# Kernel tuning notes

Measured on AMD Instinct MI355X. Metric: run time of the kernel, lower is better.

The kernel has to match this reference:

```python
import jax, jax.numpy as jnp
import numpy as np

B, T, E, H = 8, 1024, 256, 8
TEMP = E ** 0.5


def setup_inputs() -> dict:
    key = jax.random.key(0)
    ks = jax.random.split(key, 7)
    x = jax.random.normal(ks[0], (B, T, E), dtype=jnp.float32)
    # boolean mask: True = masked position (masked_fill with -inf)
    mask = jax.random.randint(ks[1], (B, T, T), 0, 2) > 0
    s_in = 1.0 / np.sqrt(E)
    s_fc = 1.0 / np.sqrt(H * E)
    Wq = jax.random.normal(ks[2], (E, H * E), dtype=jnp.float32) * s_in
    Wk = jax.random.normal(ks[3], (E, H * E), dtype=jnp.float32) * s_in
    Wv = jax.random.normal(ks[4], (E, H * E), dtype=jnp.float32) * s_in
    Wfc = jax.random.normal(ks[5], (H * E, E), dtype=jnp.float32) * s_fc
    bfc = jax.random.normal(ks[6], (E,), dtype=jnp.float32) * s_fc
    return {"x": x, "Wq": Wq, "Wk": Wk, "Wv": Wv, "Wfc": Wfc, "bfc": bfc, "mask": mask}


def reference(x, Wq, Wk, Wv, Wfc, bfc, mask):
    b, t, e = x.shape
    h = H
    # QKV projections -> [b, t, h, e] (per-head dim == emb_dim here)
    q = (x @ Wq).reshape(b, t, h, e)
    k = (x @ Wk).reshape(b, t, h, e)
    v = (x @ Wv).reshape(b, t, h, e)
    # scores: [b, h, q, k]
    attn = jnp.einsum('bqhe,bkhe->bhqk', q / TEMP, k)
    attn = jnp.where(mask[:, None, :, :], -jnp.inf, attn)
    attn = jax.nn.softmax(attn, axis=-1)
    # rows fully masked give NaN -> replaced by 0 (masked_fill(attn != attn, 0))
    attn = jnp.where(jnp.isnan(attn), 0.0, attn)
    out = jnp.einsum('bhqk,bkhe->bqhe', attn, v).reshape(b, t, h * e)
    return out @ Wfc + bfc
```

## Files before the change

kernel.cpp:

```cpp
#include <hip/hip_runtime.h>


typedef __attribute__((ext_vector_type(8))) short bf16x8;
typedef __attribute__((ext_vector_type(4))) float f32x4;
typedef __attribute__((ext_vector_type(4))) unsigned short u16x4;
typedef __attribute__((ext_vector_type(2))) unsigned int u32x2;
typedef __attribute__((ext_vector_type(4))) int i32x4;

#define B_DIM 8
#define T_DIM 1024
#define E_DIM 256
#define H_DIM 8

__device__ __forceinline__ unsigned short f2bf(float f) {
  unsigned u = __builtin_bit_cast(unsigned, f);
  u += 0x7FFFu + ((u >> 16) & 1u);
  return (unsigned short)(u >> 16);
}

__device__ __forceinline__ void gload_lds16(const void* g, void* l) {
  __builtin_amdgcn_global_load_lds(
      (const __attribute__((address_space(1))) void*)g,
      (__attribute__((address_space(3))) void*)l, 16, 0, 0);
}

__device__ __forceinline__ f32x4 mfma16(bf16x8 a, bf16x8 b, f32x4 c) {
  return __builtin_amdgcn_mfma_f32_16x16x32_bf16(a, b, c, 0, 0, 0);
}

__global__ __launch_bounds__(256) void prep_all(
    const float* __restrict__ x, unsigned short* __restrict__ xbf,
    const int* __restrict__ mask, unsigned* __restrict__ mpk,
    const float* __restrict__ Wq, const float* __restrict__ Wk,
    const float* __restrict__ Wv, const float* __restrict__ Wfc,
    unsigned short* __restrict__ wall, unsigned short* __restrict__ wfcT) {
  __shared__ unsigned short tile[64][65];
  const int bid = blockIdx.x, tid = threadIdx.x;
  if (bid < 2048) {
    int i = bid * 256 + tid;
    f32x4 v = ((const f32x4*)x)[i];
    u16x4 o = { f2bf(v[0]), f2bf(v[1]), f2bf(v[2]), f2bf(v[3]) };
    ((u16x4*)xbf)[i] = o;
    return;
  }
  if (bid < 3072) {
    int i = (bid - 2048) * 256 + tid;
    const i32x4* src = (const i32x4*)(mask + (size_t)i * 32);
    unsigned v = 0;
#pragma unroll
    for (int j = 0; j < 8; ++j) {
      i32x4 a = src[j];
      v |= (a[0] != 0 ? 1u : 0u) << (j * 4 + 0);
      v |= (a[1] != 0 ? 1u : 0u) << (j * 4 + 1);
      v |= (a[2] != 0 ? 1u : 0u) << (j * 4 + 2);
      v |= (a[3] != 0 ? 1u : 0u) << (j * 4 + 3);
    }
    mpk[i] = v;
    return;
  }
  const int which = (bid - 3072) >> 7, bx = (bid - 3072) & 127;
  const float* in;
  unsigned short* out;
  int K, N, n0, k0;
  float scale;
  if (which < 3) {
    in = which == 0 ? Wq : (which == 1 ? Wk : Wv);
    out = wall + (size_t)which * 2048 * 256;
    K = 256; N = 2048; scale = which == 2 ? 1.0f : 0.25f;
    n0 = (bx & 31) * 64; k0 = (bx >> 5) * 64;
  } else {
    in = Wfc; out = wfcT; K = 2048; N = 256; scale = 1.0f;
    n0 = (bx & 3) * 64; k0 = (bx >> 2) * 64;
  }
#pragma unroll
  for (int p = 0; p < 16; ++p) {
    int i = p * 256 + tid;
    int r = i >> 6, c = i & 63;
    tile[c][r] = f2bf(in[(size_t)(k0 + r) * N + n0 + c] * scale);
  }
  __syncthreads();
#pragma unroll
  for (int p = 0; p < 16; ++p) {
    int i = p * 256 + tid;
    int r = i >> 6, c = i & 63;
    out[(size_t)(n0 + r) * K + k0 + c] = tile[r][c];
  }
}

__global__ __launch_bounds__(512) void gemm_qkv(
    const unsigned short* __restrict__ A, const unsigned short* __restrict__ BT,
    unsigned short* __restrict__ qk, unsigned short* __restrict__ vout) {
  __shared__ unsigned short As[256 * 64];
  __shared__ unsigned short Bs[128 * 64];
  const int tid = threadIdx.x;
  const int w = tid >> 6, l = tid & 63, lg = l >> 4, lr = l & 15;
  const int tn = blockIdx.x * 128, tm = blockIdx.y * 256;
  const int wm = (w >> 1) * 64, wn = (w & 1) * 64;

  f32x4 acc[4][4];
#pragma unroll
  for (int i = 0; i < 4; ++i)
#pragma unroll
    for (int j = 0; j < 4; ++j) acc[i][j] = (f32x4){0.f, 0.f, 0.f, 0.f};

  for (int kt = 0; kt < 256; kt += 64) {
#pragma unroll
    for (int j = 0; j < 4; ++j) {
      int d = j * 8192 + tid * 16;
      int row = d >> 7, cb = d & 127;
      gload_lds16((const char*)(A + (size_t)(tm + row) * 256 + kt) + (cb ^ ((row & 7) << 4)),
                  (char*)As + d);
    }
#pragma unroll
    for (int j = 0; j < 2; ++j) {
      int d = j * 8192 + tid * 16;
      int row = d >> 7, cb = d & 127;
      gload_lds16((const char*)(BT + (size_t)(tn + row) * 256 + kt) + (cb ^ ((row & 7) << 4)),
                  (char*)Bs + d);
    }
    __syncthreads();
#pragma unroll
    for (int c = 0; c < 2; ++c) {
      bf16x8 af[4], bfr[4];
#pragma unroll
      for (int mf = 0; mf < 4; ++mf) {
        int row = wm + mf * 16 + lr;
        af[mf] = *(const bf16x8*)((const char*)As + row * 128 +
                                  ((c * 64 + lg * 16) ^ ((row & 7) << 4)));
      }
#pragma unroll
      for (int nf = 0; nf < 4; ++nf) {
        int row = wn + nf * 16 + lr;
        bfr[nf] = *(const bf16x8*)((const char*)Bs + row * 128 +
                                   ((c * 64 + lg * 16) ^ ((row & 7) << 4)));
      }
#pragma unroll
      for (int mf = 0; mf < 4; ++mf)
#pragma unroll
        for (int nf = 0; nf < 4; ++nf)
          acc[mf][nf] = mfma16(af[mf], bfr[nf], acc[mf][nf]);
    }
    __syncthreads();
  }

  if (tn < 4096) {
#pragma unroll
    for (int mf = 0; mf < 4; ++mf)
#pragma unroll
      for (int nf = 0; nf < 4; ++nf) {
        int col = tn + wn + nf * 16 + lr;
        int row0 = tm + wm + mf * 16 + lg * 4;
        int h16 = col >> 8, e = col & 255;
#pragma unroll
        for (int r = 0; r < 4; ++r) {
          int rowm = row0 + r;
          int bi = rowm >> 10, t = rowm & 1023;
          qk[(((size_t)bi * 16 + h16) * T_DIM + t) * E_DIM + e] = f2bf(acc[mf][nf][r]);
        }
      }
  } else {
#pragma unroll
    for (int mf = 0; mf < 4; ++mf)
#pragma unroll
      for (int nf = 0; nf < 4; ++nf) {
        int col = tn + wn + nf * 16 + lr;
        int row0 = tm + wm + mf * 16 + lg * 4;
        int bi = row0 >> 10, t0 = row0 & 1023;
        int hh = (col >> 8) - 16, e = col & 255;
        u16x4 pk = { f2bf(acc[mf][nf][0]), f2bf(acc[mf][nf][1]),
                     f2bf(acc[mf][nf][2]), f2bf(acc[mf][nf][3]) };
        *(u16x4*)&vout[(((size_t)bi * H_DIM + hh) * E_DIM + e) * T_DIM + t0] = pk;
      }
  }
}

__global__ __launch_bounds__(512, 2) void attn_kernel(
    const unsigned short* __restrict__ qkb, const unsigned short* __restrict__ vtb,
    const unsigned long long* __restrict__ mpk,
    unsigned short* __restrict__ aout) {
  __shared__ unsigned short Kt[64 * 256];
  __shared__ unsigned short Vt[256 * 64];
  __shared__ unsigned short Pt[8][16 * 64];

  const int tid = threadIdx.x;
  const int w = tid >> 6, l = tid & 63, lg = l >> 4, lr = l & 15;
  const int bid = blockIdx.x;
  const int x = bid & 7, j = bid >> 3;
  const int bh = x * 8 + (j >> 3), qt = j & 7;
  const int b = bh >> 3, h = bh & 7;

  const unsigned short* qg =
      qkb + (((size_t)b * 16 + h) * T_DIM + qt * 128) * E_DIM;
  const unsigned short* kg = qkb + (((size_t)b * 16 + 8 + h) * T_DIM) * E_DIM;
  const char* vgc = (const char*)(vtb + (size_t)bh * E_DIM * T_DIM);
  const unsigned long long* mrow =
      mpk + ((size_t)b * T_DIM + qt * 128 + w * 16 + lr) * 16;

  auto stageKV = [&](int kt) {
    const char* ksrc = (const char*)(kg + (size_t)(kt * 64) * E_DIM);
#pragma unroll
    for (int j2 = 0; j2 < 4; ++j2) {
      int d = j2 * 8192 + w * 1024 + l * 16;
      int row = d >> 9, cb = d & 511;
      gload_lds16(ksrc + row * 512 + (cb ^ ((row & 7) << 4)), (char*)Kt + d);
    }
#pragma unroll
    for (int j2 = 0; j2 < 4; ++j2) {
      int d = j2 * 8192 + w * 1024 + l * 16;
      int row = d >> 7, cb = d & 127;
      gload_lds16(vgc + (size_t)row * 2048 + kt * 128 + (cb ^ ((row & 7) << 4)),
                  (char*)Vt + d);
    }
  };

  stageKV(0);
  bf16x8 qf[8];
  {
    const unsigned short* qrow = qg + (size_t)(w * 16 + lr) * E_DIM + lg * 8;
#pragma unroll
    for (int c = 0; c < 8; ++c) qf[c] = *(const bf16x8*)(qrow + c * 32);
  }

  f32x4 O[16];
#pragma unroll
  for (int i = 0; i < 16; ++i) O[i] = (f32x4){0.f, 0.f, 0.f, 0.f};
  float m_run = -INFINITY, l_run = 0.f;
  unsigned long long m_cur = mrow[0];

  for (int kt = 0; kt < 16; ++kt) {
    __syncthreads();
    unsigned long long m_next = (kt < 15) ? mrow[kt + 1] : 0ull;

    f32x4 S[4];
#pragma unroll
    for (int i = 0; i < 4; ++i) S[i] = (f32x4){0.f, 0.f, 0.f, 0.f};
    __builtin_amdgcn_s_setprio(1);
#pragma unroll
    for (int kvf = 0; kvf < 4; ++kvf) {
      int row = kvf * 16 + lr;
      const char* abase = (const char*)Kt + row * 512;
      int swz = (row & 7) << 4;
#pragma unroll
      for (int c = 0; c < 8; ++c) {
        bf16x8 a = *(const bf16x8*)(abase + ((c * 64 + lg * 16) ^ swz));
        S[kvf] = mfma16(a, qf[c], S[kvf]);
      }
    }
    __builtin_amdgcn_s_setprio(0);

    float p[4][4];
    float tmax = -INFINITY;
#pragma unroll
    for (int kvf = 0; kvf < 4; ++kvf) {
      unsigned nib = (unsigned)(m_cur >> (kvf * 16 + lg * 4)) & 0xFu;
#pragma unroll
      for (int r = 0; r < 4; ++r) {
        float sv = S[kvf][r];
        if (nib & (1u << r)) sv = -INFINITY;
        p[kvf][r] = sv;
        tmax = fmaxf(tmax, sv);
      }
    }
    tmax = fmaxf(tmax, __shfl_xor(tmax, 16, 64));
    tmax = fmaxf(tmax, __shfl_xor(tmax, 32, 64));

    float m_old = m_run;
    int full = !__all(tmax - m_run <= 8.0f);
    if (full) m_run = fmaxf(m_run, tmax);
    float msafe = fmaxf(m_run, -1e30f);

    float rsum = 0.f;
#pragma unroll
    for (int kvf = 0; kvf < 4; ++kvf)
#pragma unroll
      for (int r = 0; r < 4; ++r) {
        float e = __expf(p[kvf][r] - msafe);
        p[kvf][r] = e;
        rsum += e;
      }
    rsum += __shfl_xor(rsum, 16, 64);
    rsum += __shfl_xor(rsum, 32, 64);

    if (full) {
      float alpha = __expf(m_old - msafe);
      float av0 = __shfl(alpha, lg * 4 + 0, 64);
      float av1 = __shfl(alpha, lg * 4 + 1, 64);
      float av2 = __shfl(alpha, lg * 4 + 2, 64);
      float av3 = __shfl(alpha, lg * 4 + 3, 64);
#pragma unroll
      for (int nf = 0; nf < 16; ++nf) {
        O[nf][0] *= av0; O[nf][1] *= av1; O[nf][2] *= av2; O[nf][3] *= av3;
      }
      l_run = l_run * alpha + rsum;
    } else {
      l_run += rsum;
    }

    {
      char* pb = (char*)(Pt[w]) + lr * 128;
      int swz = (lr & 7) << 4;
#pragma unroll
      for (int kvf = 0; kvf < 4; ++kvf) {
        u32x2 pk;
        pk[0] = (unsigned)f2bf(p[kvf][0]) | ((unsigned)f2bf(p[kvf][1]) << 16);
        pk[1] = (unsigned)f2bf(p[kvf][2]) | ((unsigned)f2bf(p[kvf][3]) << 16);
        *(u32x2*)(pb + ((kvf * 32 + lg * 8) ^ swz)) = pk;
      }
    }

    __builtin_amdgcn_s_setprio(1);
#pragma unroll
    for (int c2 = 0; c2 < 2; ++c2) {
      const char* pbase = (const char*)(Pt[w]) + lr * 128;
      bf16x8 pa = *(const bf16x8*)(pbase + ((c2 * 64 + lg * 16) ^ ((lr & 7) << 4)));
#pragma unroll
      for (int nf = 0; nf < 16; ++nf) {
        int vrow = nf * 16 + lr;
        bf16x8 vb = *(const bf16x8*)((const char*)Vt + vrow * 128 +
                                     ((c2 * 64 + lg * 16) ^ ((vrow & 7) << 4)));
        O[nf] = mfma16(pa, vb, O[nf]);
      }
    }
    __builtin_amdgcn_s_setprio(0);

    __syncthreads();
    if (kt < 15) { stageKV(kt + 1); m_cur = m_next; }
  }

  float lv[4];
#pragma unroll
  for (int r = 0; r < 4; ++r) {
    float lval = __shfl(l_run, lg * 4 + r, 64);
    lv[r] = lval > 0.f ? 1.f / lval : 0.f;
  }
  const int qrow0 = qt * 128 + w * 16 + lg * 4;
  unsigned short* obase = aout + (size_t)(b * T_DIM) * 2048 + h * 256;
#pragma unroll
  for (int nf = 0; nf < 16; ++nf) {
#pragma unroll
    for (int r = 0; r < 4; ++r) {
      obase[(size_t)(qrow0 + r) * 2048 + nf * 16 + lr] = f2bf(O[nf][r] * lv[r]);
    }
  }
}

__global__ __launch_bounds__(256) void gemm_fc(
    const unsigned short* __restrict__ A, const unsigned short* __restrict__ BT,
    const float* __restrict__ bias, float* __restrict__ C) {
  __shared__ unsigned short As[64 * 128];
  __shared__ unsigned short Bs[64 * 128];
  const int tid = threadIdx.x;
  const int w = tid >> 6, l = tid & 63, lg = l >> 4, lr = l & 15;
  const int tn = blockIdx.x * 64, tm = blockIdx.y * 64;
  const int wm = (w >> 1) * 32, wn = (w & 1) * 32;

  f32x4 acc[2][2];
#pragma unroll
  for (int i = 0; i < 2; ++i)
#pragma unroll
    for (int j = 0; j < 2; ++j) acc[i][j] = (f32x4){0.f, 0.f, 0.f, 0.f};

  for (int kt = 0; kt < 2048; kt += 128) {
#pragma unroll
    for (int j = 0; j < 4; ++j) {
      int d = j * 4096 + tid * 16;
      int row = d >> 8, cb = d & 255;
      gload_lds16((const char*)(A + (size_t)(tm + row) * 2048 + kt) + (cb ^ ((row & 7) << 4)),
                  (char*)As + d);
    }
#pragma unroll
    for (int j = 0; j < 4; ++j) {
      int d = j * 4096 + tid * 16;
      int row = d >> 8, cb = d & 255;
      gload_lds16((const char*)(BT + (size_t)(tn + row) * 2048 + kt) + (cb ^ ((row & 7) << 4)),
                  (char*)Bs + d);
    }
    __syncthreads();
#pragma unroll
    for (int c = 0; c < 4; ++c) {
      bf16x8 af[2], bfr[2];
#pragma unroll
      for (int mf = 0; mf < 2; ++mf) {
        int row = wm + mf * 16 + lr;
        af[mf] = *(const bf16x8*)((const char*)As + row * 256 +
                                  ((c * 64 + lg * 16) ^ ((row & 7) << 4)));
      }
#pragma unroll
      for (int nf = 0; nf < 2; ++nf) {
        int row = wn + nf * 16 + lr;
        bfr[nf] = *(const bf16x8*)((const char*)Bs + row * 256 +
                                   ((c * 64 + lg * 16) ^ ((row & 7) << 4)));
      }
#pragma unroll
      for (int mf = 0; mf < 2; ++mf)
#pragma unroll
        for (int nf = 0; nf < 2; ++nf)
          acc[mf][nf] = mfma16(af[mf], bfr[nf], acc[mf][nf]);
    }
    __syncthreads();
  }

#pragma unroll
  for (int mf = 0; mf < 2; ++mf)
#pragma unroll
    for (int nf = 0; nf < 2; ++nf) {
      int col = tn + wn + nf * 16 + lr;
      int row0 = tm + wm + mf * 16 + lg * 4;
      float bv = bias[col];
#pragma unroll
      for (int r = 0; r < 4; ++r)
        C[(size_t)(row0 + r) * 256 + col] = acc[mf][nf][r] + bv;
    }
}

extern "C" void kernel_launch(void* const* d_in, const int* in_sizes, int n_in,
                              void* d_out, int out_size, void* d_ws, size_t ws_size,
                              hipStream_t stream) {
  (void)in_sizes; (void)n_in; (void)out_size; (void)ws_size;
  const float* x    = (const float*)d_in[0];
  const float* Wq   = (const float*)d_in[1];
  const float* Wk   = (const float*)d_in[2];
  const float* Wv   = (const float*)d_in[3];
  const float* Wfc  = (const float*)d_in[4];
  const float* bfc  = (const float*)d_in[5];
  const int* mask   = (const int*)d_in[6];
  float* out = (float*)d_out;

  char* ws = (char*)d_ws;
  unsigned short* xbf  = (unsigned short*)(ws + 0);
  unsigned short* qkb  = (unsigned short*)(ws + 4194304);
  unsigned short* vbuf = (unsigned short*)(ws + 71303168);
  unsigned short* abuf = (unsigned short*)(ws + 104857600);
  unsigned short* wall = (unsigned short*)(ws + 138412032);
  unsigned short* wfcT = (unsigned short*)(ws + 141557760);
  unsigned*       mpk  = (unsigned*)(ws + 142606336);

  prep_all<<<3584, 256, 0, stream>>>(x, xbf, mask, mpk, Wq, Wk, Wv, Wfc,
                                     wall, wfcT);
  gemm_qkv<<<dim3(48, 32), 512, 0, stream>>>(xbf, wall, qkb, vbuf);
  attn_kernel<<<512, 512, 0, stream>>>(qkb, vbuf,
                                       (const unsigned long long*)mpk, abuf);
  gemm_fc<<<dim3(4, 128), 256, 0, stream>>>(abuf, wfcT, bfc, out);
}
```

Before: 290.6 us.

## Switch attention to 32x32 MFMA tiles with 32 query rows per wave

The attention kernel now uses 32x32x16 bf16 MFMA instructions, and each wave handles 32 query rows instead of 16. A block covers 256 queries, so half as many blocks stage each K/V tile, and the kernel launches 256 blocks at occupancy 1. The aim is to halve K/V LDS staging and global traffic per query and to get better operand reuse per MFMA. The cost is more registers (a 16-fragment Q, 8x16 accumulators), lower occupancy, and only 256 blocks, which may underfill 256 CUs.

```diff
diff --git a/kernel.cpp b/kernel.cpp
--- a/kernel.cpp
+++ b/kernel.cpp
@@ -3,6 +3,7 @@
 
 typedef __attribute__((ext_vector_type(8))) short bf16x8;
 typedef __attribute__((ext_vector_type(4))) float f32x4;
+typedef __attribute__((ext_vector_type(16))) float f32x16;
 typedef __attribute__((ext_vector_type(4))) unsigned short u16x4;
 typedef __attribute__((ext_vector_type(2))) unsigned int u32x2;
 typedef __attribute__((ext_vector_type(4))) int i32x4;
@@ -26,6 +27,9 @@
 
 __device__ __forceinline__ f32x4 mfma16(bf16x8 a, bf16x8 b, f32x4 c) {
   return __builtin_amdgcn_mfma_f32_16x16x32_bf16(a, b, c, 0, 0, 0);
+}
+__device__ __forceinline__ f32x16 mfma32(bf16x8 a, bf16x8 b, f32x16 c) {
+  return __builtin_amdgcn_mfma_f32_32x32x16_bf16(a, b, c, 0, 0, 0);
 }
 
 __global__ __launch_bounds__(256) void prep_all(
@@ -174,27 +178,28 @@
   }
 }
 
-__global__ __launch_bounds__(512, 2) void attn_kernel(
+__global__ __launch_bounds__(512, 1) void attn_kernel(
     const unsigned short* __restrict__ qkb, const unsigned short* __restrict__ vtb,
     const unsigned long long* __restrict__ mpk,
     unsigned short* __restrict__ aout) {
   __shared__ unsigned short Kt[64 * 256];
   __shared__ unsigned short Vt[256 * 64];
-  __shared__ unsigned short Pt[8][16 * 64];
+  __shared__ unsigned short Pt[8][32 * 64];
 
   const int tid = threadIdx.x;
-  const int w = tid >> 6, l = tid & 63, lg = l >> 4, lr = l & 15;
+  const int w = tid >> 6, l = tid & 63;
+  const int q32 = l & 31, hi = l >> 5;
   const int bid = blockIdx.x;
   const int x = bid & 7, j = bid >> 3;
-  const int bh = x * 8 + (j >> 3), qt = j & 7;
+  const int bh = x * 8 + (j >> 2), qt = j & 3;
   const int b = bh >> 3, h = bh & 7;
 
   const unsigned short* qg =
-      qkb + (((size_t)b * 16 + h) * T_DIM + qt * 128) * E_DIM;
+      qkb + (((size_t)b * 16 + h) * T_DIM + qt * 256) * E_DIM;
   const unsigned short* kg = qkb + (((size_t)b * 16 + 8 + h) * T_DIM) * E_DIM;
   const char* vgc = (const char*)(vtb + (size_t)bh * E_DIM * T_DIM);
   const unsigned long long* mrow =
-      mpk + ((size_t)b * T_DIM + qt * 128 + w * 16 + lr) * 16;
+      mpk + ((size_t)b * T_DIM + qt * 256 + w * 32 + q32) * 16;
 
   auto stageKV = [&](int kt) {
     const char* ksrc = (const char*)(kg + (size_t)(kt * 64) * E_DIM);
@@ -214,16 +219,16 @@
   };
 
   stageKV(0);
-  bf16x8 qf[8];
+  bf16x8 qf[16];
   {
-    const unsigned short* qrow = qg + (size_t)(w * 16 + lr) * E_DIM + lg * 8;
-#pragma unroll
-    for (int c = 0; c < 8; ++c) qf[c] = *(const bf16x8*)(qrow + c * 32);
-  }
-
-  f32x4 O[16];
-#pragma unroll
-  for (int i = 0; i < 16; ++i) O[i] = (f32x4){0.f, 0.f, 0.f, 0.f};
+    const unsigned short* qrow = qg + (size_t)(w * 32 + q32) * E_DIM + hi * 8;
+#pragma unroll
+    for (int e = 0; e < 16; ++e) qf[e] = *(const bf16x8*)(qrow + e * 16);
+  }
+
+  f32x16 O[8];
+#pragma unroll
+  for (int i = 0; i < 8; ++i) O[i] = (f32x16)(0.f);
   float m_run = -INFINITY, l_run = 0.f;
   unsigned long long m_cur = mrow[0];
 
@@ -231,37 +236,33 @@
     __syncthreads();
     unsigned long long m_next = (kt < 15) ? mrow[kt + 1] : 0ull;
 
-    f32x4 S[4];
-#pragma unroll
-    for (int i = 0; i < 4; ++i) S[i] = (f32x4){0.f, 0.f, 0.f, 0.f};
+    f32x16 S0 = (f32x16)(0.f), S1 = (f32x16)(0.f);
     __builtin_amdgcn_s_setprio(1);
 #pragma unroll
-    for (int kvf = 0; kvf < 4; ++kvf) {
-      int row = kvf * 16 + lr;
-      const char* abase = (const char*)Kt + row * 512;
-      int swz = (row & 7) << 4;
-#pragma unroll
-      for (int c = 0; c < 8; ++c) {
-        bf16x8 a = *(const bf16x8*)(abase + ((c * 64 + lg * 16) ^ swz));
-        S[kvf] = mfma16(a, qf[c], S[kvf]);
-      }
+    for (int e = 0; e < 16; ++e) {
+      int eb = e * 32 + hi * 16;
+      bf16x8 a0 = *(const bf16x8*)((const char*)Kt + q32 * 512 +
+                                   (eb ^ ((q32 & 7) << 4)));
+      S0 = mfma32(a0, qf[e], S0);
+      int row1 = 32 + q32;
+      bf16x8 a1 = *(const bf16x8*)((const char*)Kt + row1 * 512 +
+                                   (eb ^ ((row1 & 7) << 4)));
+      S1 = mfma32(a1, qf[e], S1);
     }
     __builtin_amdgcn_s_setprio(0);
 
-    float p[4][4];
+    float p0[16], p1[16];
     float tmax = -INFINITY;
-#pragma unroll
-    for (int kvf = 0; kvf < 4; ++kvf) {
-      unsigned nib = (unsigned)(m_cur >> (kvf * 16 + lg * 4)) & 0xFu;
-#pragma unroll
-      for (int r = 0; r < 4; ++r) {
-        float sv = S[kvf][r];
-        if (nib & (1u << r)) sv = -INFINITY;
-        p[kvf][r] = sv;
-        tmax = fmaxf(tmax, sv);
-      }
-    }
-    tmax = fmaxf(tmax, __shfl_xor(tmax, 16, 64));
+    unsigned long long mm = m_cur >> (4 * hi);
+#pragma unroll
+    for (int r = 0; r < 16; ++r) {
+      const int cr = (r & 3) + 8 * (r >> 2);
+      float s0 = S0[r], s1 = S1[r];
+      if ((mm >> cr) & 1ull) s0 = -INFINITY;
+      if ((mm >> (cr + 32)) & 1ull) s1 = -INFINITY;
+      p0[r] = s0; p1[r] = s1;
+      tmax = fmaxf(tmax, fmaxf(s0, s1));
+    }
     tmax = fmaxf(tmax, __shfl_xor(tmax, 32, 64));
 
     float m_old = m_run;
@@ -271,54 +272,62 @@
 
     float rsum = 0.f;
 #pragma unroll
-    for (int kvf = 0; kvf < 4; ++kvf)
-#pragma unroll
-      for (int r = 0; r < 4; ++r) {
-        float e = __expf(p[kvf][r] - msafe);
-        p[kvf][r] = e;
-        rsum += e;
-      }
-    rsum += __shfl_xor(rsum, 16, 64);
+    for (int r = 0; r < 16; ++r) {
+      float e0 = __expf(p0[r] - msafe);
+      float e1 = __expf(p1[r] - msafe);
+      p0[r] = e0; p1[r] = e1;
+      rsum += e0 + e1;
+    }
     rsum += __shfl_xor(rsum, 32, 64);
 
     if (full) {
       float alpha = __expf(m_old - msafe);
-      float av0 = __shfl(alpha, lg * 4 + 0, 64);
-      float av1 = __shfl(alpha, lg * 4 + 1, 64);
-      float av2 = __shfl(alpha, lg * 4 + 2, 64);
-      float av3 = __shfl(alpha, lg * 4 + 3, 64);
-#pragma unroll
-      for (int nf = 0; nf < 16; ++nf) {
-        O[nf][0] *= av0; O[nf][1] *= av1; O[nf][2] *= av2; O[nf][3] *= av3;
-      }
+      float av[16];
+#pragma unroll
+      for (int r = 0; r < 16; ++r)
+        av[r] = __shfl(alpha, (r & 3) + 8 * (r >> 2) + 4 * hi, 64);
+#pragma unroll
+      for (int nf = 0; nf < 8; ++nf)
+#pragma unroll
+        for (int r = 0; r < 16; ++r) O[nf][r] *= av[r];
       l_run = l_run * alpha + rsum;
     } else {
       l_run += rsum;
     }
 
     {
-      char* pb = (char*)(Pt[w]) + lr * 128;
-      int swz = (lr & 7) << 4;
-#pragma unroll
-      for (int kvf = 0; kvf < 4; ++kvf) {
-        u32x2 pk;
-        pk[0] = (unsigned)f2bf(p[kvf][0]) | ((unsigned)f2bf(p[kvf][1]) << 16);
-        pk[1] = (unsigned)f2bf(p[kvf][2]) | ((unsigned)f2bf(p[kvf][3]) << 16);
-        *(u32x2*)(pb + ((kvf * 32 + lg * 8) ^ swz)) = pk;
+      char* pb = (char*)(Pt[w]) + q32 * 128;
+      const int swz = (q32 & 7) << 4;
+#pragma unroll
+      for (int g = 0; g < 4; ++g) {
+        u32x2 k0, k1;
+        k0[0] = (unsigned)f2bf(p0[g * 4 + 0]) | ((unsigned)f2bf(p0[g * 4 + 1]) << 16);
+        k0[1] = (unsigned)f2bf(p0[g * 4 + 2]) | ((unsigned)f2bf(p0[g * 4 + 3]) << 16);
+        *(u32x2*)(pb + ((g * 16 + hi * 8) ^ swz)) = k0;
+        k1[0] = (unsigned)f2bf(p1[g * 4 + 0]) | ((unsigned)f2bf(p1[g * 4 + 1]) << 16);
+        k1[1] = (unsigned)f2bf(p1[g * 4 + 2]) | ((unsigned)f2bf(p1[g * 4 + 3]) << 16);
+        *(u32x2*)(pb + ((g * 16 + hi * 8 + 64) ^ swz)) = k1;
       }
     }
 
     __builtin_amdgcn_s_setprio(1);
-#pragma unroll
-    for (int c2 = 0; c2 < 2; ++c2) {
-      const char* pbase = (const char*)(Pt[w]) + lr * 128;
-      bf16x8 pa = *(const bf16x8*)(pbase + ((c2 * 64 + lg * 16) ^ ((lr & 7) << 4)));
-#pragma unroll
-      for (int nf = 0; nf < 16; ++nf) {
-        int vrow = nf * 16 + lr;
-        bf16x8 vb = *(const bf16x8*)((const char*)Vt + vrow * 128 +
-                                     ((c2 * 64 + lg * 16) ^ ((vrow & 7) << 4)));
-        O[nf] = mfma16(pa, vb, O[nf]);
+    {
+      const char* pbr = (const char*)(Pt[w]) + q32 * 128;
+      const int swz = (q32 & 7) << 4;
+      bf16x8 pa[4];
+#pragma unroll
+      for (int ks = 0; ks < 4; ++ks)
+        pa[ks] = *(const bf16x8*)(pbr + ((ks * 32 + hi * 16) ^ swz));
+#pragma unroll
+      for (int nf = 0; nf < 8; ++nf) {
+        int vrow = nf * 32 + q32;
+        const char* vbase = (const char*)Vt + vrow * 128;
+        const int vswz = (vrow & 7) << 4;
+#pragma unroll
+        for (int ks = 0; ks < 4; ++ks) {
+          bf16x8 vb = *(const bf16x8*)(vbase + ((ks * 32 + hi * 16) ^ vswz));
+          O[nf] = mfma32(pa[ks], vb, O[nf]);
+        }
       }
     }
     __builtin_amdgcn_s_setprio(0);
@@ -327,19 +336,19 @@
     if (kt < 15) { stageKV(kt + 1); m_cur = m_next; }
   }
 
-  float lv[4];
-#pragma unroll
-  for (int r = 0; r < 4; ++r) {
-    float lval = __shfl(l_run, lg * 4 + r, 64);
-    lv[r] = lval > 0.f ? 1.f / lval : 0.f;
-  }
-  const int qrow0 = qt * 128 + w * 16 + lg * 4;
+  float linv = l_run > 0.f ? 1.f / l_run : 0.f;
+  float lv[16];
+#pragma unroll
+  for (int r = 0; r < 16; ++r)
+    lv[r] = __shfl(linv, (r & 3) + 8 * (r >> 2) + 4 * hi, 64);
   unsigned short* obase = aout + (size_t)(b * T_DIM) * 2048 + h * 256;
-#pragma unroll
-  for (int nf = 0; nf < 16; ++nf) {
-#pragma unroll
-    for (int r = 0; r < 4; ++r) {
-      obase[(size_t)(qrow0 + r) * 2048 + nf * 16 + lr] = f2bf(O[nf][r] * lv[r]);
+  const int q0 = qt * 256 + w * 32 + 4 * hi;
+#pragma unroll
+  for (int nf = 0; nf < 8; ++nf) {
+#pragma unroll
+    for (int r = 0; r < 16; ++r) {
+      int qrow = q0 + (r & 3) + 8 * (r >> 2);
+      obase[(size_t)qrow * 2048 + nf * 32 + q32] = f2bf(O[nf][r] * lv[r]);
     }
   }
 }
@@ -438,7 +447,7 @@
   prep_all<<<3584, 256, 0, stream>>>(x, xbf, mask, mpk, Wq, Wk, Wv, Wfc,
                                      wall, wfcT);
   gemm_qkv<<<dim3(48, 32), 512, 0, stream>>>(xbf, wall, qkb, vbuf);
-  attn_kernel<<<512, 512, 0, stream>>>(qkb, vbuf,
+  attn_kernel<<<256, 512, 0, stream>>>(qkb, vbuf,
                                        (const unsigned long long*)mpk, abuf);
   gemm_fc<<<dim3(4, 128), 256, 0, stream>>>(abuf, wfcT, bfc, out);
 }
```

New measurement: 368.3 us. 26.7% more time.

## Process two 16-row query groups per wave in attention kernel with 4 waves

Applied to the files above, without the earlier changes.

The attention kernel now runs 256 threads (4 waves) per block instead of 8, with each wave handling 32 query rows as two 16-row groups. Each K or V fragment read from LDS is reused for two MFMAs, halving LDS read traffic per FLOP. The cost is doubled accumulator and register state per wave (O is 2x16 f32x4), and launch bounds drop to one block per CU target, which can lower occupancy and latency hiding.

```diff
diff --git a/kernel.cpp b/kernel.cpp
--- a/kernel.cpp
+++ b/kernel.cpp
@@ -174,13 +174,13 @@
   }
 }
 
-__global__ __launch_bounds__(512, 2) void attn_kernel(
+__global__ __launch_bounds__(256, 1) void attn_kernel(
     const unsigned short* __restrict__ qkb, const unsigned short* __restrict__ vtb,
     const unsigned long long* __restrict__ mpk,
     unsigned short* __restrict__ aout) {
   __shared__ unsigned short Kt[64 * 256];
   __shared__ unsigned short Vt[256 * 64];
-  __shared__ unsigned short Pt[8][16 * 64];
+  __shared__ unsigned short Pt[4][32 * 64];
 
   const int tid = threadIdx.x;
   const int w = tid >> 6, l = tid & 63, lg = l >> 4, lr = l & 15;
@@ -193,20 +193,21 @@
       qkb + (((size_t)b * 16 + h) * T_DIM + qt * 128) * E_DIM;
   const unsigned short* kg = qkb + (((size_t)b * 16 + 8 + h) * T_DIM) * E_DIM;
   const char* vgc = (const char*)(vtb + (size_t)bh * E_DIM * T_DIM);
-  const unsigned long long* mrow =
-      mpk + ((size_t)b * T_DIM + qt * 128 + w * 16 + lr) * 16;
+  const unsigned long long* mrow0 =
+      mpk + ((size_t)b * T_DIM + qt * 128 + w * 32 + lr) * 16;
+  const unsigned long long* mrow1 = mrow0 + 16 * 16;
 
   auto stageKV = [&](int kt) {
     const char* ksrc = (const char*)(kg + (size_t)(kt * 64) * E_DIM);
 #pragma unroll
-    for (int j2 = 0; j2 < 4; ++j2) {
-      int d = j2 * 8192 + w * 1024 + l * 16;
+    for (int p = 0; p < 8; ++p) {
+      int d = p * 4096 + tid * 16;
       int row = d >> 9, cb = d & 511;
       gload_lds16(ksrc + row * 512 + (cb ^ ((row & 7) << 4)), (char*)Kt + d);
     }
 #pragma unroll
-    for (int j2 = 0; j2 < 4; ++j2) {
-      int d = j2 * 8192 + w * 1024 + l * 16;
+    for (int p = 0; p < 8; ++p) {
+      int d = p * 4096 + tid * 16;
       int row = d >> 7, cb = d & 127;
       gload_lds16(vgc + (size_t)row * 2048 + kt * 128 + (cb ^ ((row & 7) << 4)),
                   (char*)Vt + d);
@@ -214,26 +215,35 @@
   };
 
   stageKV(0);
-  bf16x8 qf[8];
-  {
-    const unsigned short* qrow = qg + (size_t)(w * 16 + lr) * E_DIM + lg * 8;
-#pragma unroll
-    for (int c = 0; c < 8; ++c) qf[c] = *(const bf16x8*)(qrow + c * 32);
-  }
-
-  f32x4 O[16];
-#pragma unroll
-  for (int i = 0; i < 16; ++i) O[i] = (f32x4){0.f, 0.f, 0.f, 0.f};
-  float m_run = -INFINITY, l_run = 0.f;
-  unsigned long long m_cur = mrow[0];
+  bf16x8 qf[2][8];
+#pragma unroll
+  for (int g = 0; g < 2; ++g) {
+    const unsigned short* qrow =
+        qg + (size_t)(w * 32 + g * 16 + lr) * E_DIM + lg * 8;
+#pragma unroll
+    for (int c = 0; c < 8; ++c) qf[g][c] = *(const bf16x8*)(qrow + c * 32);
+  }
+
+  f32x4 O[2][16];
+#pragma unroll
+  for (int g = 0; g < 2; ++g)
+#pragma unroll
+    for (int i = 0; i < 16; ++i) O[g][i] = (f32x4){0.f, 0.f, 0.f, 0.f};
+  float m_run0 = -INFINITY, m_run1 = -INFINITY;
+  float l_run0 = 0.f, l_run1 = 0.f;
+  unsigned long long mc0 = mrow0[0], mc1 = mrow1[0];
 
   for (int kt = 0; kt < 16; ++kt) {
     __syncthreads();
-    unsigned long long m_next = (kt < 15) ? mrow[kt + 1] : 0ull;
-
-    f32x4 S[4];
-#pragma unroll
-    for (int i = 0; i < 4; ++i) S[i] = (f32x4){0.f, 0.f, 0.f, 0.f};
+    unsigned long long mn0 = (kt < 15) ? mrow0[kt + 1] : 0ull;
+    unsigned long long mn1 = (kt < 15) ? mrow1[kt + 1] : 0ull;
+
+    f32x4 S0[4], S1[4];
+#pragma unroll
+    for (int i = 0; i < 4; ++i) {
+      S0[i] = (f32x4){0.f, 0.f, 0.f, 0.f};
+      S1[i] = (f32x4){0.f, 0.f, 0.f, 0.f};
+    }
     __builtin_amdgcn_s_setprio(1);
 #pragma unroll
     for (int kvf = 0; kvf < 4; ++kvf) {
@@ -243,103 +253,135 @@
 #pragma unroll
       for (int c = 0; c < 8; ++c) {
         bf16x8 a = *(const bf16x8*)(abase + ((c * 64 + lg * 16) ^ swz));
-        S[kvf] = mfma16(a, qf[c], S[kvf]);
+        S0[kvf] = mfma16(a, qf[0][c], S0[kvf]);
+        S1[kvf] = mfma16(a, qf[1][c], S1[kvf]);
       }
     }
     __builtin_amdgcn_s_setprio(0);
 
-    float p[4][4];
-    float tmax = -INFINITY;
+    float p0[4][4], p1[4][4];
+    float tmax0 = -INFINITY, tmax1 = -INFINITY;
 #pragma unroll
     for (int kvf = 0; kvf < 4; ++kvf) {
-      unsigned nib = (unsigned)(m_cur >> (kvf * 16 + lg * 4)) & 0xFu;
+      unsigned nib0 = (unsigned)(mc0 >> (kvf * 16 + lg * 4)) & 0xFu;
+      unsigned nib1 = (unsigned)(mc1 >> (kvf * 16 + lg * 4)) & 0xFu;
 #pragma unroll
       for (int r = 0; r < 4; ++r) {
-        float sv = S[kvf][r];
-        if (nib & (1u << r)) sv = -INFINITY;
-        p[kvf][r] = sv;
-        tmax = fmaxf(tmax, sv);
-      }
-    }
-    tmax = fmaxf(tmax, __shfl_xor(tmax, 16, 64));
-    tmax = fmaxf(tmax, __shfl_xor(tmax, 32, 64));
-
-    float m_old = m_run;
-    int full = !__all(tmax - m_run <= 8.0f);
-    if (full) m_run = fmaxf(m_run, tmax);
-    float msafe = fmaxf(m_run, -1e30f);
-
-    float rsum = 0.f;
+        float s0 = S0[kvf][r], s1 = S1[kvf][r];
+        if (nib0 & (1u << r)) s0 = -INFINITY;
+        if (nib1 & (1u << r)) s1 = -INFINITY;
+        p0[kvf][r] = s0; p1[kvf][r] = s1;
+        tmax0 = fmaxf(tmax0, s0); tmax1 = fmaxf(tmax1, s1);
+      }
+    }
+    tmax0 = fmaxf(tmax0, __shfl_xor(tmax0, 16, 64));
+    tmax0 = fmaxf(tmax0, __shfl_xor(tmax0, 32, 64));
+    tmax1 = fmaxf(tmax1, __shfl_xor(tmax1, 16, 64));
+    tmax1 = fmaxf(tmax1, __shfl_xor(tmax1, 32, 64));
+
+    float m_old0 = m_run0, m_old1 = m_run1;
+    int full = !__all(fmaxf(tmax0 - m_run0, tmax1 - m_run1) <= 8.0f);
+    if (full) { m_run0 = fmaxf(m_run0, tmax0); m_run1 = fmaxf(m_run1, tmax1); }
+    float ms0 = fmaxf(m_run0, -1e30f), ms1 = fmaxf(m_run1, -1e30f);
+
+    float rs0 = 0.f, rs1 = 0.f;
 #pragma unroll
     for (int kvf = 0; kvf < 4; ++kvf)
 #pragma unroll
       for (int r = 0; r < 4; ++r) {
-        float e = __expf(p[kvf][r] - msafe);
-        p[kvf][r] = e;
-        rsum += e;
-      }
-    rsum += __shfl_xor(rsum, 16, 64);
-    rsum += __shfl_xor(rsum, 32, 64);
+        float e0 = __expf(p0[kvf][r] - ms0);
+        float e1 = __expf(p1[kvf][r] - ms1);
+        p0[kvf][r] = e0; p1[kvf][r] = e1;
+        rs0 += e0; rs1 += e1;
+      }
+    rs0 += __shfl_xor(rs0, 16, 64);
+    rs0 += __shfl_xor(rs0, 32, 64);
+    rs1 += __shfl_xor(rs1, 16, 64);
+    rs1 += __shfl_xor(rs1, 32, 64);
 
     if (full) {
-      float alpha = __expf(m_old - msafe);
-      float av0 = __shfl(alpha, lg * 4 + 0, 64);
-      float av1 = __shfl(alpha, lg * 4 + 1, 64);
-      float av2 = __shfl(alpha, lg * 4 + 2, 64);
-      float av3 = __shfl(alpha, lg * 4 + 3, 64);
-#pragma unroll
-      for (int nf = 0; nf < 16; ++nf) {
-        O[nf][0] *= av0; O[nf][1] *= av1; O[nf][2] *= av2; O[nf][3] *= av3;
-      }
-      l_run = l_run * alpha + rsum;
+      float a0 = __expf(m_old0 - ms0), a1 = __expf(m_old1 - ms1);
+      float av0[4], av1[4];
+#pragma unroll
+      for (int r = 0; r < 4; ++r) {
+        av0[r] = __shfl(a0, lg * 4 + r, 64);
+        av1[r] = __shfl(a1, lg * 4 + r, 64);
+      }
+#pragma unroll
+      for (int nf = 0; nf < 16; ++nf)
+#pragma unroll
+        for (int r = 0; r < 4; ++r) {
+          O[0][nf][r] *= av0[r];
+          O[1][nf][r] *= av1[r];
+        }
+      l_run0 = l_run0 * a0 + rs0;
+      l_run1 = l_run1 * a1 + rs1;
     } else {
-      l_run += rsum;
+      l_run0 += rs0;
+      l_run1 += rs1;
     }
 
     {
-      char* pb = (char*)(Pt[w]) + lr * 128;
-      int swz = (lr & 7) << 4;
-#pragma unroll
-      for (int kvf = 0; kvf < 4; ++kvf) {
-        u32x2 pk;
-        pk[0] = (unsigned)f2bf(p[kvf][0]) | ((unsigned)f2bf(p[kvf][1]) << 16);
-        pk[1] = (unsigned)f2bf(p[kvf][2]) | ((unsigned)f2bf(p[kvf][3]) << 16);
-        *(u32x2*)(pb + ((kvf * 32 + lg * 8) ^ swz)) = pk;
+      const int swz = (lr & 7) << 4;
+#pragma unroll
+      for (int g = 0; g < 2; ++g) {
+        char* pb = (char*)(Pt[w]) + (g * 16 + lr) * 128;
+        const float(*pg)[4] = g ? p1 : p0;
+#pragma unroll
+        for (int kvf = 0; kvf < 4; ++kvf) {
+          u32x2 pk;
+          pk[0] = (unsigned)f2bf(pg[kvf][0]) | ((unsigned)f2bf(pg[kvf][1]) << 16);
+          pk[1] = (unsigned)f2bf(pg[kvf][2]) | ((unsigned)f2bf(pg[kvf][3]) << 16);
+          *(u32x2*)(pb + ((kvf * 32 + lg * 8) ^ swz)) = pk;
+        }
       }
     }
 
     __builtin_amdgcn_s_setprio(1);
-#pragma unroll
-    for (int c2 = 0; c2 < 2; ++c2) {
-      const char* pbase = (const char*)(Pt[w]) + lr * 128;
-      bf16x8 pa = *(const bf16x8*)(pbase + ((c2 * 64 + lg * 16) ^ ((lr & 7) << 4)));
-#pragma unroll
-      for (int nf = 0; nf < 16; ++nf) {
-        int vrow = nf * 16 + lr;
-        bf16x8 vb = *(const bf16x8*)((const char*)Vt + vrow * 128 +
-                                     ((c2 * 64 + lg * 16) ^ ((vrow & 7) << 4)));
-        O[nf] = mfma16(pa, vb, O[nf]);
+    {
+      const int swz = (lr & 7) << 4;
+      bf16x8 pa0[2], pa1[2];
+#pragma unroll
+      for (int c2 = 0; c2 < 2; ++c2) {
+        pa0[c2] = *(const bf16x8*)((const char*)(Pt[w]) + (0 * 16 + lr) * 128 +
+                                   ((c2 * 64 + lg * 16) ^ swz));
+        pa1[c2] = *(const bf16x8*)((const char*)(Pt[w]) + (1 * 16 + lr) * 128 +
+                                   ((c2 * 64 + lg * 16) ^ swz));
+      }
+#pragma unroll
+      for (int c2 = 0; c2 < 2; ++c2) {
+#pragma unroll
+        for (int nf = 0; nf < 16; ++nf) {
+          int vrow = nf * 16 + lr;
+          bf16x8 vb = *(const bf16x8*)((const char*)Vt + vrow * 128 +
+                                       ((c2 * 64 + lg * 16) ^ ((vrow & 7) << 4)));
+          O[0][nf] = mfma16(pa0[c2], vb, O[0][nf]);
+          O[1][nf] = mfma16(pa1[c2], vb, O[1][nf]);
+        }
       }
     }
     __builtin_amdgcn_s_setprio(0);
 
     __syncthreads();
-    if (kt < 15) { stageKV(kt + 1); m_cur = m_next; }
-  }
-
-  float lv[4];
+    if (kt < 15) { stageKV(kt + 1); mc0 = mn0; mc1 = mn1; }
+  }
+
+  float li0 = l_run0 > 0.f ? 1.f / l_run0 : 0.f;
+  float li1 = l_run1 > 0.f ? 1.f / l_run1 : 0.f;
+  float lv0[4], lv1[4];
 #pragma unroll
   for (int r = 0; r < 4; ++r) {
-    float lval = __shfl(l_run, lg * 4 + r, 64);
-    lv[r] = lval > 0.f ? 1.f / lval : 0.f;
-  }
-  const int qrow0 = qt * 128 + w * 16 + lg * 4;
+    lv0[r] = __shfl(li0, lg * 4 + r, 64);
+    lv1[r] = __shfl(li1, lg * 4 + r, 64);
+  }
   unsigned short* obase = aout + (size_t)(b * T_DIM) * 2048 + h * 256;
+  const int q0 = qt * 128 + w * 32 + lg * 4;
 #pragma unroll
   for (int nf = 0; nf < 16; ++nf) {
 #pragma unroll
     for (int r = 0; r < 4; ++r) {
-      obase[(size_t)(qrow0 + r) * 2048 + nf * 16 + lr] = f2bf(O[nf][r] * lv[r]);
+      obase[(size_t)(q0 + r) * 2048 + nf * 16 + lr] = f2bf(O[0][nf][r] * lv0[r]);
+      obase[(size_t)(q0 + 16 + r) * 2048 + nf * 16 + lr] = f2bf(O[1][nf][r] * lv1[r]);
     }
   }
 }
@@ -438,7 +480,7 @@
   prep_all<<<3584, 256, 0, stream>>>(x, xbf, mask, mpk, Wq, Wk, Wv, Wfc,
                                      wall, wfcT);
   gemm_qkv<<<dim3(48, 32), 512, 0, stream>>>(xbf, wall, qkb, vbuf);
-  attn_kernel<<<512, 512, 0, stream>>>(qkb, vbuf,
+  attn_kernel<<<512, 256, 0, stream>>>(qkb, vbuf,
                                        (const unsigned long long*)mpk, abuf);
   gemm_fc<<<dim3(4, 128), 256, 0, stream>>>(abuf, wfcT, bfc, out);
 }
```

Measured after the change: 331.7 us. 14.1% more time.
